# Kernel tuning notes

Measured on AMD Instinct MI355X. Metric: run time of the kernel, lower is better.

The kernel has to match this reference:

```python
import jax, jax.numpy as jnp
import numpy as np

N_NODES = 50000
N_EDGES = 800000
IN_FEAT = 256
DIM_H = 64
DIM_OUT = 64


def setup_inputs() -> dict:
    key = jax.random.key(0)
    ks = jax.random.split(key, 9)
    x = jax.random.normal(ks[0], (N_NODES, IN_FEAT), dtype=jnp.float32)
    edge_index = jax.random.randint(ks[1], (2, N_EDGES), 0, N_NODES, dtype=jnp.int64)
    s_in = 1.0 / np.sqrt(IN_FEAT)
    s_h = 1.0 / np.sqrt(DIM_H)
    W_src = jax.random.normal(ks[2], (IN_FEAT, DIM_H), dtype=jnp.float32) * s_in
    W_dst = jax.random.normal(ks[3], (IN_FEAT, DIM_H), dtype=jnp.float32) * s_in
    att_src = jax.random.normal(ks[4], (DIM_H,), dtype=jnp.float32) * s_h
    att_dst = jax.random.normal(ks[5], (DIM_H,), dtype=jnp.float32) * s_h
    bias_conv = jax.random.normal(ks[6], (DIM_H,), dtype=jnp.float32) * 0.01
    W_lin = jax.random.normal(ks[7], (DIM_H, DIM_OUT), dtype=jnp.float32) * s_h
    b_lin = jax.random.normal(ks[8], (DIM_OUT,), dtype=jnp.float32) * 0.01
    return {"x": x, "edge_index": edge_index, "W_src": W_src, "W_dst": W_dst,
            "att_src": att_src, "att_dst": att_dst, "bias_conv": bias_conv,
            "W_lin": W_lin, "b_lin": b_lin}


def reference(x, edge_index, W_src, W_dst, att_src, att_dst, bias_conv, W_lin, b_lin):
    N = x.shape[0]
    src, dst = edge_index[0], edge_index[1]
    # linear projections (GATConv lin_src / lin_dst, no bias)
    h_src = x @ W_src                      # [N, H]
    h_dst = x @ W_dst                      # [N, H]
    # per-node attention logits
    a_src = h_src @ att_src                # [N]
    a_dst = h_dst @ att_dst                # [N]
    # edge-wise score: leaky_relu(a_src[src] + a_dst[dst])
    e = jax.nn.leaky_relu(a_src[src] + a_dst[dst], negative_slope=0.2)  # [E]
    # segment softmax over destination neighborhoods
    e_max = jax.ops.segment_max(e, dst, num_segments=N)
    e_exp = jnp.exp(e - e_max[dst])
    denom = jax.ops.segment_sum(e_exp, dst, num_segments=N)
    alpha = e_exp / denom[dst]             # [E]
    # weighted scatter-add aggregation
    msg = h_src[src] * alpha[:, None]      # [E, H]
    out = jax.ops.segment_sum(msg, dst, num_segments=N) + bias_conv  # [N, H]
    h = jax.nn.relu(out)
    return h @ W_lin + b_lin               # [N, dim_out]
```

## Files before the change

### kernel.cpp

```cpp
#include <hip/hip_runtime.h>
#include <math.h>

#define N_NODES 50000
#define N_EDGES 800000
#define IN_FEAT 256
#define DIM_H   64
#define NPAD    50176
#define CAP     48
#define NBUK2   1568
#define BCAP2   768
#define EPB     4096
#define PBLKS   784
#define ABLKS   196
#define PNODES  32

typedef __attribute__((ext_vector_type(8)))  short  s16x8;
typedef __attribute__((ext_vector_type(16))) float  f32x16;

__device__ __forceinline__ float bcast_f(float v, int k) {
  return __int_as_float(__builtin_amdgcn_readlane(__float_as_int(v), k));
}
__device__ __forceinline__ short f2bf(float f) {
  unsigned u = __float_as_uint(f);
  u += 0x7fffu + ((u >> 16) & 1u);
  return (short)(u >> 16);
}

__global__ __launch_bounds__(256, 4) void proj_binA_kernel(
    const float* __restrict__ x,
    const float* __restrict__ Wsrc,
    const float* __restrict__ Wdst,
    const float* __restrict__ att_src,
    const float* __restrict__ att_dst,
    const int* __restrict__ ei,
    unsigned* __restrict__ hbf,
    float* __restrict__ a_src,
    float* __restrict__ a_dst,
    int* __restrict__ gbc,
    unsigned* __restrict__ binbuf) {
  __shared__ short wfrag[16 * 2 * 64 * 8];
  __shared__ float wdl[IN_FEAT];
  __shared__ float attl[DIM_H];

  const int tid = threadIdx.x;

  if (blockIdx.x >= PBLKS) {
    int* bcnt = (int*)wfrag;
    int* wcur = bcnt + NBUK2;
    const int e0 = (blockIdx.x - PBLKS) * EPB;

    for (int b = tid; b < NBUK2; b += 256) bcnt[b] = 0;
    __syncthreads();

    int dst[16];
    #pragma unroll
    for (int i = 0; i < 16; ++i) {
      int e = e0 + tid + 256 * i;
      dst[i] = (e < N_EDGES) ? ei[N_EDGES + e] : -1;
      if (dst[i] >= 0) atomicAdd(&bcnt[dst[i] >> 5], 1);
    }
    __syncthreads();

    for (int b = tid; b < NBUK2; b += 256) {
      int c = bcnt[b];
      wcur[b] = c ? atomicAdd(&gbc[b], c) : 0;
    }
    __syncthreads();

    #pragma unroll
    for (int i = 0; i < 16; ++i) {
      int e = e0 + tid + 256 * i;
      if (e < N_EDGES) {
        int s = ei[e];
        int b = dst[i] >> 5;
        int pos = atomicAdd(&wcur[b], 1);
        if (pos < BCAP2)
          binbuf[(long)b * BCAP2 + pos] =
              (unsigned)s | ((unsigned)(dst[i] & 31) << 16);
      }
    }
    return;
  }

  const int lane = tid & 63;
  const int wv   = tid >> 6;
  const int tile = wv >> 1;
  const int h    = wv & 1;

  if (tid < DIM_H) attl[tid] = att_dst[tid];
  __syncthreads();

  {
    float s = 0.f;
    const float4* row = (const float4*)(Wdst + (long)tid * DIM_H);
    #pragma unroll
    for (int q = 0; q < 16; ++q) {
      float4 r = row[q];
      s = fmaf(r.x, attl[4 * q + 0], s);
      s = fmaf(r.y, attl[4 * q + 1], s);
      s = fmaf(r.z, attl[4 * q + 2], s);
      s = fmaf(r.w, attl[4 * q + 3], s);
    }
    wdl[tid] = s;
  }

  for (int e4 = tid * 4; e4 < IN_FEAT * DIM_H; e4 += 1024) {
    float4 w4 = *(const float4*)(Wsrc + e4);
    int k = e4 >> 6, n0 = e4 & 63;
    int s = k >> 4, half = (k >> 3) & 1, j = k & 7, t = n0 >> 5;
    short* p = &wfrag[((s * 2 + t) * 64 + ((n0 & 31) + 32 * half)) * 8 + j];
    p[0]  = f2bf(w4.x);
    p[8]  = f2bf(w4.y);
    p[16] = f2bf(w4.z);
    p[24] = f2bf(w4.w);
  }
  __syncthreads();

  const int base  = blockIdx.x * 64 + tile * 32;
  int row = base + (lane & 31); if (row > N_NODES - 1) row = N_NODES - 1;
  const int koff8 = (lane >> 5) * 8;
  const int k0    = h * 128;
  const float* px = x + (long)row * IN_FEAT + k0 + koff8;

  f32x16 acc0, acc1;
  #pragma unroll
  for (int i = 0; i < 16; ++i) { acc0[i] = 0.f; acc1[i] = 0.f; }
  float pd = 0.f;

  #pragma unroll
  for (int s = 0; s < 8; ++s) {
    float4 va = *(const float4*)(px + s * 16);
    float4 vb = *(const float4*)(px + s * 16 + 4);
    const float* wp = wdl + k0 + s * 16 + koff8;
    float4 w1 = *(const float4*)(wp);
    float4 w2 = *(const float4*)(wp + 4);
    pd = fmaf(va.x, w1.x, pd); pd = fmaf(va.y, w1.y, pd);
    pd = fmaf(va.z, w1.z, pd); pd = fmaf(va.w, w1.w, pd);
    pd = fmaf(vb.x, w2.x, pd); pd = fmaf(vb.y, w2.y, pd);
    pd = fmaf(vb.z, w2.z, pd); pd = fmaf(vb.w, w2.w, pd);
    s16x8 a;
    a[0] = f2bf(va.x); a[1] = f2bf(va.y); a[2] = f2bf(va.z); a[3] = f2bf(va.w);
    a[4] = f2bf(vb.x); a[5] = f2bf(vb.y); a[6] = f2bf(vb.z); a[7] = f2bf(vb.w);
    const int f = (h * 8 + s) * 2;
    s16x8 b0 = *(const s16x8*)(wfrag + ((f + 0) * 64 + lane) * 8);
    s16x8 b1 = *(const s16x8*)(wfrag + ((f + 1) * 64 + lane) * 8);
    acc0 = __builtin_amdgcn_mfma_f32_32x32x16_bf16(a, b0, acc0, 0, 0, 0);
    acc1 = __builtin_amdgcn_mfma_f32_32x32x16_bf16(a, b1, acc1, 0, 0, 0);
  }
  float pds = pd + __shfl_xor(pd, 32, 64);

  __syncthreads();
  float* fa = (float*)wfrag;
  float* myslot = fa + tile * 2304 + lane * 36;
  float* pdb    = fa + 4608 + tile * 32;

  if (h == 1) {
    #pragma unroll
    for (int i = 0; i < 4; ++i)
      *(float4*)(myslot + i * 4) =
          make_float4(acc0[4 * i], acc0[4 * i + 1], acc0[4 * i + 2], acc0[4 * i + 3]);
    #pragma unroll
    for (int i = 0; i < 4; ++i)
      *(float4*)(myslot + 16 + i * 4) =
          make_float4(acc1[4 * i], acc1[4 * i + 1], acc1[4 * i + 2], acc1[4 * i + 3]);
    if (lane < 32) pdb[lane] = pds;
  }
  __syncthreads();
  if (h == 1) return;

  #pragma unroll
  for (int i = 0; i < 4; ++i) {
    float4 t = *(const float4*)(myslot + i * 4);
    acc0[4 * i] += t.x; acc0[4 * i + 1] += t.y;
    acc0[4 * i + 2] += t.z; acc0[4 * i + 3] += t.w;
  }
  #pragma unroll
  for (int i = 0; i < 4; ++i) {
    float4 t = *(const float4*)(myslot + 16 + i * 4);
    acc1[4 * i] += t.x; acc1[4 * i + 1] += t.y;
    acc1[4 * i + 2] += t.z; acc1[4 * i + 3] += t.w;
  }
  pds += pdb[lane & 31];

  const int col = lane & 31;
  const int rhi = 4 * (lane >> 5);

  #pragma unroll
  for (int r = 0; r < 16; ++r) {
    int node = base + (r & 3) + 8 * (r >> 2) + rhi;
    if (node < N_NODES) {
      unsigned p = (unsigned)(unsigned short)f2bf(acc0[r]) |
                   ((unsigned)(unsigned short)f2bf(acc1[r]) << 16);
      hbf[(long)node * 32 + col] = p;
    }
  }

  float att0 = att_src[col];
  float att1 = att_src[col + 32];
  #pragma unroll
  for (int r = 0; r < 16; ++r) {
    float t = acc0[r] * att0 + acc1[r] * att1;
    t += __shfl_xor(t, 1, 64);
    t += __shfl_xor(t, 2, 64);
    t += __shfl_xor(t, 4, 64);
    t += __shfl_xor(t, 8, 64);
    t += __shfl_xor(t, 16, 64);
    int node = base + (r & 3) + 8 * (r >> 2) + rhi;
    if (col == 0 && node < N_NODES) a_src[node] = t;
  }

  int node = base + (lane & 31);
  if (lane < 32 && node < N_NODES) a_dst[node] = pds;
}

__global__ __launch_bounds__(256) void gatherfused_kernel(
    const unsigned* __restrict__ binbuf,
    const int* __restrict__ gbc,
    const float* __restrict__ a_src,
    const float* __restrict__ a_dst,
    const unsigned* __restrict__ hbf,
    const float* __restrict__ bias_conv,
    const float* __restrict__ W_lin,
    const float* __restrict__ b_lin,
    float* __restrict__ out) {
  __shared__ unsigned rec[PNODES * CAP];
  __shared__ int   lcnt[PNODES];
  __shared__ float adl[PNODES];
  __shared__ float wl[64 * 64];

  const int tid    = threadIdx.x;
  const int bucket = blockIdx.x;
  const int nb     = bucket * PNODES;

  {
    const float4* wsrc4 = (const float4*)W_lin;
    float4* wl4 = (float4*)wl;
    for (int i = tid; i < 1024; i += 256) wl4[i] = wsrc4[i];
  }
  if (tid < PNODES) {
    lcnt[tid] = 0;
    adl[tid]  = a_dst[nb + tid];
  }
  __syncthreads();

  int count = gbc[bucket]; if (count > BCAP2) count = BCAP2;
  const unsigned* bb = binbuf + (long)bucket * BCAP2;
  for (int i = tid; i < count; i += 256) {
    unsigned u = bb[i];
    int dl = (int)(u >> 16);
    int s  = (int)(u & 0xffffu);
    float sc = a_src[s] + adl[dl];
    sc = sc >= 0.f ? sc : 0.2f * sc;
    float w = __expf(sc);
    int pos = atomicAdd(&lcnt[dl], 1);
    if (pos < CAP)
      rec[dl * CAP + pos] =
          ((unsigned)(unsigned short)f2bf(w) << 16) | (u & 0xffffu);
  }
  __syncthreads();

  const int lane = tid & 63;
  const int wv   = __builtin_amdgcn_readfirstlane(tid >> 6);
  const int grp8 = lane >> 3;
  const int ql8  = lane & 7;
  const float bj  = bias_conv[lane];
  const float blj = b_lin[lane];

  for (int q = 0; q < 8; ++q) {
    const int dl = wv * 8 + q;
    const int n  = nb + dl;
    int m = lcnt[dl]; if (m > CAP) m = CAP;

    float alo[4] = {0.f, 0.f, 0.f, 0.f};
    float ahi[4] = {0.f, 0.f, 0.f, 0.f};
    float den = 0.f;

    for (int j = 0; j < m; j += 16) {
      int idx0 = j + grp8;
      int idx1 = j + 8 + grp8;
      int ci0 = idx0 < m ? idx0 : m - 1;
      int ci1 = idx1 < m ? idx1 : m - 1;
      unsigned u0 = rec[dl * CAP + ci0];
      unsigned u1 = rec[dl * CAP + ci1];
      float w0 = __uint_as_float(u0 & 0xffff0000u);
      float w1 = __uint_as_float(u1 & 0xffff0000u);
      if (idx0 >= m) w0 = 0.f;
      if (idx1 >= m) w1 = 0.f;
      int s0 = (int)(u0 & 0xffffu);
      int s1 = (int)(u1 & 0xffffu);
      uint4 hp0 = *(const uint4*)(hbf + (long)s0 * 32 + ql8 * 4);
      uint4 hp1 = *(const uint4*)(hbf + (long)s1 * 32 + ql8 * 4);
      alo[0] = fmaf(w0, __uint_as_float(hp0.x << 16),         alo[0]);
      ahi[0] = fmaf(w0, __uint_as_float(hp0.x & 0xffff0000u), ahi[0]);
      alo[1] = fmaf(w0, __uint_as_float(hp0.y << 16),         alo[1]);
      ahi[1] = fmaf(w0, __uint_as_float(hp0.y & 0xffff0000u), ahi[1]);
      alo[2] = fmaf(w0, __uint_as_float(hp0.z << 16),         alo[2]);
      ahi[2] = fmaf(w0, __uint_as_float(hp0.z & 0xffff0000u), ahi[2]);
      alo[3] = fmaf(w0, __uint_as_float(hp0.w << 16),         alo[3]);
      ahi[3] = fmaf(w0, __uint_as_float(hp0.w & 0xffff0000u), ahi[3]);
      den += w0;
      alo[0] = fmaf(w1, __uint_as_float(hp1.x << 16),         alo[0]);
      ahi[0] = fmaf(w1, __uint_as_float(hp1.x & 0xffff0000u), ahi[0]);
      alo[1] = fmaf(w1, __uint_as_float(hp1.y << 16),         alo[1]);
      ahi[1] = fmaf(w1, __uint_as_float(hp1.y & 0xffff0000u), ahi[1]);
      alo[2] = fmaf(w1, __uint_as_float(hp1.z << 16),         alo[2]);
      ahi[2] = fmaf(w1, __uint_as_float(hp1.z & 0xffff0000u), ahi[2]);
      alo[3] = fmaf(w1, __uint_as_float(hp1.w << 16),         alo[3]);
      ahi[3] = fmaf(w1, __uint_as_float(hp1.w & 0xffff0000u), ahi[3]);
      den += w1;
    }

    #pragma unroll
    for (int mm = 8; mm <= 32; mm <<= 1) {
      #pragma unroll
      for (int c = 0; c < 4; ++c) {
        alo[c] += __shfl_xor(alo[c], mm, 64);
        ahi[c] += __shfl_xor(ahi[c], mm, 64);
      }
      den += __shfl_xor(den, mm, 64);
    }
    int srcl = (lane & 31) >> 2;
    float v0 = __shfl(alo[0], srcl, 64);
    float v1 = __shfl(alo[1], srcl, 64);
    float v2 = __shfl(alo[2], srcl, 64);
    float v3 = __shfl(alo[3], srcl, 64);
    float v4 = __shfl(ahi[0], srcl, 64);
    float v5 = __shfl(ahi[1], srcl, 64);
    float v6 = __shfl(ahi[2], srcl, 64);
    float v7 = __shfl(ahi[3], srcl, 64);
    int c4 = lane & 3;
    float losel = (c4 == 0) ? v0 : (c4 == 1) ? v1 : (c4 == 2) ? v2 : v3;
    float hisel = (c4 == 0) ? v4 : (c4 == 1) ? v5 : (c4 == 2) ? v6 : v7;
    float accl = (lane >> 5) ? hisel : losel;

    float inv = den > 0.f ? 1.0f / den : 0.f;
    float z = fmaf(accl, inv, bj);
    float h = fmaxf(z, 0.f);
    float o0 = blj, o1 = 0.f, o2 = 0.f, o3 = 0.f;
    #pragma unroll
    for (int k = 0; k < 64; k += 4) {
      o0 = fmaf(bcast_f(h, k + 0), wl[(k + 0) * 64 + lane], o0);
      o1 = fmaf(bcast_f(h, k + 1), wl[(k + 1) * 64 + lane], o1);
      o2 = fmaf(bcast_f(h, k + 2), wl[(k + 2) * 64 + lane], o2);
      o3 = fmaf(bcast_f(h, k + 3), wl[(k + 3) * 64 + lane], o3);
    }
    float o = (o0 + o1) + (o2 + o3);
    if (n < N_NODES) out[(long)n * DIM_H + lane] = o;
  }
}

extern "C" void kernel_launch(void* const* d_in, const int* in_sizes, int n_in,
                              void* d_out, int out_size, void* d_ws, size_t ws_size,
                              hipStream_t stream) {
  const float* x        = (const float*)d_in[0];
  const int*   ei       = (const int*)d_in[1];
  const float* Wsrc     = (const float*)d_in[2];
  const float* Wdst     = (const float*)d_in[3];
  const float* att_src  = (const float*)d_in[4];
  const float* att_dst  = (const float*)d_in[5];
  const float* bias_cv  = (const float*)d_in[6];
  const float* W_lin    = (const float*)d_in[7];
  const float* b_lin    = (const float*)d_in[8];
  float* out = (float*)d_out;

  unsigned* hbf    = (unsigned*)d_ws;
  float*    a_src  = (float*)(hbf + 1600000);
  float*    a_dst  = a_src + NPAD;
  int*      gbc    = (int*)(a_dst + NPAD);
  unsigned* binbuf = (unsigned*)(gbc + 2048);

  hipMemsetAsync(gbc, 0, 2048 * sizeof(int), stream);

  proj_binA_kernel<<<PBLKS + ABLKS, 256, 0, stream>>>(
      x, Wsrc, Wdst, att_src, att_dst, ei, hbf, a_src, a_dst, gbc, binbuf);

  gatherfused_kernel<<<NBUK2, 256, 0, stream>>>(
      binbuf, gbc, a_src, a_dst, hbf, bias_cv, W_lin, b_lin, out);
}
```

Measured before the change: 171.4 us.

## Precompute weight fragments in prep kernel and prefetch next node's gather

Adds a single-block prep kernel that zeroes the bucket counters and computes the Wdst·att_dst vector and the bf16 MFMA-layout Wsrc fragments once. The projection blocks then copy these precomputed tables instead of redoing the conversion in every block, and the prep kernel replaces the memset. In the gather kernel, the first 16 neighbours of the next destination node are prefetched while the current node is processed, to hide gather latency. The cost is an extra kernel launch with one serial block and more register pressure in the gather loop.

```diff
diff --git a/kernel.cpp b/kernel.cpp
--- a/kernel.cpp
+++ b/kernel.cpp
@@ -26,12 +26,52 @@
   return (short)(u >> 16);
 }
 
+__global__ __launch_bounds__(256) void prep_kernel(
+    const float* __restrict__ Wsrc,
+    const float* __restrict__ Wdst,
+    const float* __restrict__ att_dst,
+    float* __restrict__ wdl_g,
+    short* __restrict__ wfrag_g,
+    int* __restrict__ gbc) {
+  __shared__ float attl[DIM_H];
+  const int tid = threadIdx.x;
+
+  for (int i = tid; i < 2048; i += 256) gbc[i] = 0;
+
+  if (tid < DIM_H) attl[tid] = att_dst[tid];
+  __syncthreads();
+
+  {
+    float s = 0.f;
+    const float4* row = (const float4*)(Wdst + (long)tid * DIM_H);
+    #pragma unroll
+    for (int q = 0; q < 16; ++q) {
+      float4 r = row[q];
+      s = fmaf(r.x, attl[4 * q + 0], s);
+      s = fmaf(r.y, attl[4 * q + 1], s);
+      s = fmaf(r.z, attl[4 * q + 2], s);
+      s = fmaf(r.w, attl[4 * q + 3], s);
+    }
+    wdl_g[tid] = s;
+  }
+
+  for (int e4 = tid * 4; e4 < IN_FEAT * DIM_H; e4 += 1024) {
+    float4 w4 = *(const float4*)(Wsrc + e4);
+    int k = e4 >> 6, n0 = e4 & 63;
+    int sg = k >> 4, half = (k >> 3) & 1, j = k & 7, t = n0 >> 5;
+    short* p = &wfrag_g[((sg * 2 + t) * 64 + ((n0 & 31) + 32 * half)) * 8 + j];
+    p[0]  = f2bf(w4.x);
+    p[8]  = f2bf(w4.y);
+    p[16] = f2bf(w4.z);
+    p[24] = f2bf(w4.w);
+  }
+}
+
 __global__ __launch_bounds__(256, 4) void proj_binA_kernel(
     const float* __restrict__ x,
-    const float* __restrict__ Wsrc,
-    const float* __restrict__ Wdst,
+    const float* __restrict__ wdl_g,
+    const short* __restrict__ wfrag_g,
     const float* __restrict__ att_src,
-    const float* __restrict__ att_dst,
     const int* __restrict__ ei,
     unsigned* __restrict__ hbf,
     float* __restrict__ a_src,
@@ -40,7 +80,6 @@
     unsigned* __restrict__ binbuf) {
   __shared__ short wfrag[16 * 2 * 64 * 8];
   __shared__ float wdl[IN_FEAT];
-  __shared__ float attl[DIM_H];
 
   const int tid = threadIdx.x;
 
@@ -87,32 +126,11 @@
   const int tile = wv >> 1;
   const int h    = wv & 1;
 
-  if (tid < DIM_H) attl[tid] = att_dst[tid];
-  __syncthreads();
-
+  if (tid < 64) ((float4*)wdl)[tid] = ((const float4*)wdl_g)[tid];
   {
-    float s = 0.f;
-    const float4* row = (const float4*)(Wdst + (long)tid * DIM_H);
-    #pragma unroll
-    for (int q = 0; q < 16; ++q) {
-      float4 r = row[q];
-      s = fmaf(r.x, attl[4 * q + 0], s);
-      s = fmaf(r.y, attl[4 * q + 1], s);
-      s = fmaf(r.z, attl[4 * q + 2], s);
-      s = fmaf(r.w, attl[4 * q + 3], s);
-    }
-    wdl[tid] = s;
-  }
-
-  for (int e4 = tid * 4; e4 < IN_FEAT * DIM_H; e4 += 1024) {
-    float4 w4 = *(const float4*)(Wsrc + e4);
-    int k = e4 >> 6, n0 = e4 & 63;
-    int s = k >> 4, half = (k >> 3) & 1, j = k & 7, t = n0 >> 5;
-    short* p = &wfrag[((s * 2 + t) * 64 + ((n0 & 31) + 32 * half)) * 8 + j];
-    p[0]  = f2bf(w4.x);
-    p[8]  = f2bf(w4.y);
-    p[16] = f2bf(w4.z);
-    p[24] = f2bf(w4.w);
+    uint4* d = (uint4*)wfrag;
+    const uint4* s4 = (const uint4*)wfrag_g;
+    for (int i = tid; i < 2048; i += 256) d[i] = s4[i];
   }
   __syncthreads();
 
@@ -266,16 +284,64 @@
   const float bj  = bias_conv[lane];
   const float blj = b_lin[lane];
 
+  auto prefetch = [&](int dl, int m_, float& W0, float& W1, uint4& HP0, uint4& HP1) {
+    if (m_ > 0) {
+      int i0 = (grp8     < m_) ? grp8     : m_ - 1;
+      int i1 = (8 + grp8 < m_) ? 8 + grp8 : m_ - 1;
+      unsigned u0 = rec[dl * CAP + i0];
+      unsigned u1 = rec[dl * CAP + i1];
+      W0 = (grp8     < m_) ? __uint_as_float(u0 & 0xffff0000u) : 0.f;
+      W1 = (8 + grp8 < m_) ? __uint_as_float(u1 & 0xffff0000u) : 0.f;
+      HP0 = *(const uint4*)(hbf + (long)(u0 & 0xffffu) * 32 + ql8 * 4);
+      HP1 = *(const uint4*)(hbf + (long)(u1 & 0xffffu) * 32 + ql8 * 4);
+    } else {
+      W0 = 0.f; W1 = 0.f;
+      HP0 = make_uint4(0u, 0u, 0u, 0u);
+      HP1 = make_uint4(0u, 0u, 0u, 0u);
+    }
+  };
+
+  int mcur = lcnt[wv * 8]; if (mcur > CAP) mcur = CAP;
+  float pw0, pw1; uint4 php0, php1;
+  prefetch(wv * 8, mcur, pw0, pw1, php0, php1);
+
+  #pragma unroll
   for (int q = 0; q < 8; ++q) {
     const int dl = wv * 8 + q;
     const int n  = nb + dl;
-    int m = lcnt[dl]; if (m > CAP) m = CAP;
+    const int m  = mcur;
 
     float alo[4] = {0.f, 0.f, 0.f, 0.f};
     float ahi[4] = {0.f, 0.f, 0.f, 0.f};
     float den = 0.f;
 
-    for (int j = 0; j < m; j += 16) {
+    {
+      alo[0] = fmaf(pw0, __uint_as_float(php0.x << 16),         alo[0]);
+      ahi[0] = fmaf(pw0, __uint_as_float(php0.x & 0xffff0000u), ahi[0]);
+      alo[1] = fmaf(pw0, __uint_as_float(php0.y << 16),         alo[1]);
+      ahi[1] = fmaf(pw0, __uint_as_float(php0.y & 0xffff0000u), ahi[1]);
+      alo[2] = fmaf(pw0, __uint_as_float(php0.z << 16),         alo[2]);
+      ahi[2] = fmaf(pw0, __uint_as_float(php0.z & 0xffff0000u), ahi[2]);
+      alo[3] = fmaf(pw0, __uint_as_float(php0.w << 16),         alo[3]);
+      ahi[3] = fmaf(pw0, __uint_as_float(php0.w & 0xffff0000u), ahi[3]);
+      den += pw0;
+      alo[0] = fmaf(pw1, __uint_as_float(php1.x << 16),         alo[0]);
+      ahi[0] = fmaf(pw1, __uint_as_float(php1.x & 0xffff0000u), ahi[0]);
+      alo[1] = fmaf(pw1, __uint_as_float(php1.y << 16),         alo[1]);
+      ahi[1] = fmaf(pw1, __uint_as_float(php1.y & 0xffff0000u), ahi[1]);
+      alo[2] = fmaf(pw1, __uint_as_float(php1.z << 16),         alo[2]);
+      ahi[2] = fmaf(pw1, __uint_as_float(php1.z & 0xffff0000u), ahi[2]);
+      alo[3] = fmaf(pw1, __uint_as_float(php1.w << 16),         alo[3]);
+      ahi[3] = fmaf(pw1, __uint_as_float(php1.w & 0xffff0000u), ahi[3]);
+      den += pw1;
+    }
+
+    if (q < 7) {
+      mcur = lcnt[dl + 1]; if (mcur > CAP) mcur = CAP;
+      prefetch(dl + 1, mcur, pw0, pw1, php0, php1);
+    }
+
+    for (int j = 16; j < m; j += 16) {
       int idx0 = j + grp8;
       int idx1 = j + 8 + grp8;
       int ci0 = idx0 < m ? idx0 : m - 1;
@@ -335,14 +401,14 @@
 
     float inv = den > 0.f ? 1.0f / den : 0.f;
     float z = fmaf(accl, inv, bj);
-    float h = fmaxf(z, 0.f);
+    float hh = fmaxf(z, 0.f);
     float o0 = blj, o1 = 0.f, o2 = 0.f, o3 = 0.f;
     #pragma unroll
     for (int k = 0; k < 64; k += 4) {
-      o0 = fmaf(bcast_f(h, k + 0), wl[(k + 0) * 64 + lane], o0);
-      o1 = fmaf(bcast_f(h, k + 1), wl[(k + 1) * 64 + lane], o1);
-      o2 = fmaf(bcast_f(h, k + 2), wl[(k + 2) * 64 + lane], o2);
-      o3 = fmaf(bcast_f(h, k + 3), wl[(k + 3) * 64 + lane], o3);
+      o0 = fmaf(bcast_f(hh, k + 0), wl[(k + 0) * 64 + lane], o0);
+      o1 = fmaf(bcast_f(hh, k + 1), wl[(k + 1) * 64 + lane], o1);
+      o2 = fmaf(bcast_f(hh, k + 2), wl[(k + 2) * 64 + lane], o2);
+      o3 = fmaf(bcast_f(hh, k + 3), wl[(k + 3) * 64 + lane], o3);
     }
     float o = (o0 + o1) + (o2 + o3);
     if (n < N_NODES) out[(long)n * DIM_H + lane] = o;
@@ -368,11 +434,13 @@
   float*    a_dst  = a_src + NPAD;
   int*      gbc    = (int*)(a_dst + NPAD);
   unsigned* binbuf = (unsigned*)(gbc + 2048);
-
-  hipMemsetAsync(gbc, 0, 2048 * sizeof(int), stream);
+  float*    wdl_g  = (float*)(binbuf + (long)NBUK2 * BCAP2);
+  short*    wfrag_g = (short*)(wdl_g + 256);
+
+  prep_kernel<<<1, 256, 0, stream>>>(Wsrc, Wdst, att_dst, wdl_g, wfrag_g, gbc);
 
   proj_binA_kernel<<<PBLKS + ABLKS, 256, 0, stream>>>(
-      x, Wsrc, Wdst, att_src, att_dst, ei, hbf, a_src, a_dst, gbc, binbuf);
+      x, wdl_g, wfrag_g, att_src, ei, hbf, a_src, a_dst, gbc, binbuf);
 
   gatherfused_kernel<<<NBUK2, 256, 0, stream>>>(
       binbuf, gbc, a_src, a_dst, hbf, bias_cv, W_lin, b_lin, out);
```

New measurement: 176.9 us. +3.2%, slower.
